# Optimization experiments

Measured on AMD Instinct MI355X. Metric: run time of the kernel, lower is better.

## Reference

```python
import jax, jax.numpy as jnp
import numpy as np

K, PAD, POOL = 3, 1, 2

def _conv_block(x, w, b):
    # x: [B,C,H,W]; w: [O, C*K*K] (Linear weight, feature order (C,kh,kw)); b: [O]
    O = w.shape[0]
    C = x.shape[1]
    ker = w.reshape(O, C, K, K)  # OIHW, matches torch unfold+linear ordering
    y = jax.lax.conv_general_dilated(
        x, ker, window_strides=(1, 1), padding=[(PAD, PAD), (PAD, PAD)],
        dimension_numbers=("NCHW", "OIHW", "NCHW"))
    y = y + b[None, :, None, None]
    y = jax.nn.relu(y)
    # non-overlapping max pool, drops remainder like torch unfold (sizes divisible here)
    y = jax.lax.reduce_window(y, -jnp.inf, jax.lax.max,
                              (1, 1, POOL, POOL), (1, 1, POOL, POOL), "VALID")
    return y

def setup_inputs() -> dict:
    key = jax.random.key(0)
    ks = jax.random.split(key, 9)
    B, Cin, H = 64, 3, 128
    C1, C2, FC, NCLS = 64, 128, 256, 1000
    flat = C2 * (H // 4) * (H // 4)  # 128*32*32 = 131072
    s = 0.05
    return {
        "x": jax.random.normal(ks[0], (B, Cin, H, H), jnp.float32),
        "conv1_w": jax.random.normal(ks[1], (C1, Cin * K * K), jnp.float32) * s,
        "conv1_b": jax.random.normal(ks[2], (C1,), jnp.float32) * s,
        "conv2_w": jax.random.normal(ks[3], (C2, C1 * K * K), jnp.float32) * s,
        "conv2_b": jax.random.normal(ks[4], (C2,), jnp.float32) * s,
        "fc1_w": jax.random.normal(ks[5], (FC, flat), jnp.float32) * 0.005,
        "fc1_b": jax.random.normal(ks[6], (FC,), jnp.float32) * s,
        "fc2_w": jax.random.normal(ks[7], (NCLS, FC), jnp.float32) * s,
        "fc2_b": jax.random.normal(ks[8], (NCLS,), jnp.float32) * s,
    }

def reference(x, conv1_w, conv1_b, conv2_w, conv2_b, fc1_w, fc1_b, fc2_w, fc2_b):
    h = _conv_block(x, conv1_w, conv1_b)      # [B,64,64,64]
    h = _conv_block(h, conv2_w, conv2_b)      # [B,128,32,32]
    h = h.reshape(h.shape[0], -1)             # NCHW flatten, same as torch .view
    h = jax.nn.relu(h @ fc1_w.T + fc1_b)
    return h @ fc2_w.T + fc2_b                # [B,1000]
```

## Files before the change

kernel.cpp:

```cpp
#include <hip/hip_runtime.h>
#include <hip/hip_bf16.h>

typedef __attribute__((ext_vector_type(8))) short short8;
typedef __attribute__((ext_vector_type(4))) float f32x4;

#define KFC   131072
#define NCLS  1000

__device__ __forceinline__ unsigned short f2bf(float f) {
  union { float f; unsigned u; } v; v.f = f;
  unsigned r = v.u + 0x7FFFu + ((v.u >> 16) & 1u);
  return (unsigned short)(r >> 16);
}

__device__ __forceinline__ unsigned pk2bf(float a, float b) {
  __hip_bfloat162 h = __float22bfloat162_rn(float2{a, b});
  union { __hip_bfloat162 h; unsigned u; } c; c.h = h;
  return c.u;
}

__global__ __launch_bounds__(256) void prep_w1(
    const float* __restrict__ w1, short* __restrict__ Bp1) {
  int i = blockIdx.x * 256 + threadIdx.x;
  int o = i >> 5, k = i & 31;
  Bp1[i] = (k < 27) ? (short)f2bf(w1[o * 27 + k]) : (short)0;
}

__global__ __launch_bounds__(256) void conv1_mfma(
    const float* __restrict__ x, const short* __restrict__ Bp1,
    const float* __restrict__ b1, unsigned short* __restrict__ y) {
  __shared__ unsigned short tile[1152];
  const int t = threadIdx.x;
  const int blk = blockIdx.x;
  const int tx = blk & 7, ty = (blk >> 3) & 7, b = blk >> 6;
  const int w = t >> 6, lane = t & 63;
  const int l15 = lane & 15, lg = lane >> 4;

  const int ih0 = ty * 16 - 1, iw0 = tx * 16 - 1;
  for (int i = t; i < 1152; i += 256) {
    unsigned short v = 0;
    if (i < 1080) {
      int ci = i / 360, rem = i - ci * 360;
      int tr = rem / 20, tc = rem - tr * 20;
      int ih = ih0 + tr, iw = iw0 + tc;
      if (tc < 18 && (unsigned)ih < 128u && (unsigned)iw < 128u)
        v = f2bf(x[(b * 3 + ci) * 16384 + (ih << 7) + iw]);
    }
    tile[i] = v;
  }

  short8 bf[4];
#pragma unroll
  for (int n = 0; n < 4; ++n)
    bf[n] = *(const short8*)(Bp1 + ((n * 16 + l15) << 5) + (lg << 3));

  int soff[8];
#pragma unroll
  for (int j = 0; j < 8; ++j) {
    int k = lg * 8 + j;
    if (k < 27) {
      int ci = k / 9, rem = k - ci * 9;
      int r = rem / 3, s = rem - r * 3;
      soff[j] = ci * 360 + r * 20 + s + l15 + w * 80;
    } else {
      soff[j] = 1080;
    }
  }
  __syncthreads();

  f32x4 acc[4][4];
#pragma unroll
  for (int m = 0; m < 4; ++m)
#pragma unroll
    for (int n = 0; n < 4; ++n) acc[m][n] = (f32x4){0.f, 0.f, 0.f, 0.f};

#pragma unroll
  for (int m = 0; m < 4; ++m) {
    union { short8 s; unsigned short u[8]; } af;
#pragma unroll
    for (int j = 0; j < 8; ++j) af.u[j] = tile[soff[j] + m * 20];
#pragma unroll
    for (int n = 0; n < 4; ++n)
      acc[m][n] = __builtin_amdgcn_mfma_f32_16x16x32_bf16(af.s, bf[n], acc[m][n], 0, 0, 0);
  }

#pragma unroll
  for (int n = 0; n < 4; ++n) {
    const int o = n * 16 + l15;
    const float bias = b1[o];
#pragma unroll
    for (int q = 0; q < 2; ++q) {
      const int pr = ty * 8 + w * 2 + q;
      float v0 = fmaxf(fmaxf(acc[2 * q][n][0], acc[2 * q][n][1]),
                       fmaxf(acc[2 * q + 1][n][0], acc[2 * q + 1][n][1]));
      float v1 = fmaxf(fmaxf(acc[2 * q][n][2], acc[2 * q][n][3]),
                       fmaxf(acc[2 * q + 1][n][2], acc[2 * q + 1][n][3]));
      v0 = fmaxf(v0 + bias, 0.f);
      v1 = fmaxf(v1 + bias, 0.f);
      const int pc = tx * 8 + lg * 2;
      unsigned short* dst = y + ((((size_t)b << 6) + pr) << 12) + ((size_t)pc << 6) + o;
      dst[0]  = f2bf(v0);
      dst[64] = f2bf(v1);
    }
  }
}

__global__ __launch_bounds__(256) void prep_w2(
    const float* __restrict__ w2, short* __restrict__ Bp) {
  int i = blockIdx.x * 256 + threadIdx.x;
  int c = i & 31, o = (i >> 5) & 127, pp = i >> 12;
  int cg = pp / 9, pos = pp - cg * 9;
  Bp[i] = (short)f2bf(w2[o * 576 + (cg * 32 + c) * 9 + pos]);
}

__global__ __launch_bounds__(512) void conv2_mfma(
    const short* __restrict__ yin, const short* __restrict__ Bp,
    const float* __restrict__ b2, unsigned int* __restrict__ A32) {
  __shared__ short tile[324 * 40];
  const int t = threadIdx.x;
  const int blk = blockIdx.x;
  const int tx = blk & 3, ty = (blk >> 2) & 3, b = blk >> 4;
  const int w = t >> 6, lane = t & 63;
  const int wm = w & 1, wn = w >> 1;
  const int l15 = lane & 15, lg = lane >> 4;

  f32x4 acc[8][2];
#pragma unroll
  for (int m = 0; m < 8; ++m)
#pragma unroll
    for (int n = 0; n < 2; ++n) acc[m][n] = (f32x4){0.f, 0.f, 0.f, 0.f};

  const int ih0 = ty * 16 - 1, iw0 = tx * 16 - 1;

#pragma unroll
  for (int cg = 0; cg < 2; ++cg) {
    __syncthreads();
    for (int i = t; i < 324 * 4; i += 512) {
      int p = i >> 2, q = i & 3;
      int sy = p / 18, sx = p - sy * 18;
      int ih = ih0 + sy, iw = iw0 + sx;
      short8 v = (short8){0, 0, 0, 0, 0, 0, 0, 0};
      if (((unsigned)ih < 64u) && ((unsigned)iw < 64u))
        v = *(const short8*)(yin + ((((size_t)b << 6) + ih) << 12) + ((size_t)iw << 6) + cg * 32 + q * 8);
      *(short8*)&tile[p * 40 + q * 8] = v;
    }
    __syncthreads();

    const int py0 = wm * 8;
#pragma unroll
    for (int pos = 0; pos < 9; ++pos) {
      const int kh = pos / 3, kw = pos % 3;
      short8 bf[2];
#pragma unroll
      for (int n = 0; n < 2; ++n)
        bf[n] = *(const short8*)(Bp + ((((cg * 9 + pos) << 7) + (wn * 2 + n) * 16 + l15) << 5) + (lg << 3));
#pragma unroll
      for (int half = 0; half < 2; ++half) {
        short8 af[4];
#pragma unroll
        for (int m = 0; m < 4; ++m) {
          int sy = py0 + half * 4 + m + kh, sx = l15 + kw;
          af[m] = *(const short8*)&tile[(sy * 18 + sx) * 40 + lg * 8];
        }
#pragma unroll
        for (int n = 0; n < 2; ++n)
#pragma unroll
          for (int m = 0; m < 4; ++m)
            acc[half * 4 + m][n] = __builtin_amdgcn_mfma_f32_16x16x32_bf16(af[m], bf[n], acc[half * 4 + m][n], 0, 0, 0);
      }
    }
  }

  const size_t bbase = ((size_t)b << 16);
#pragma unroll
  for (int n = 0; n < 2; ++n) {
    const int o = (wn * 2 + n) * 16 + l15;
    const float bias = b2[o];
#pragma unroll
    for (int mp = 0; mp < 4; ++mp) {
      const int prow = ty * 8 + wm * 4 + mp;
      float v0 = fmaxf(fmaxf(acc[2 * mp][n][0], acc[2 * mp][n][1]),
                       fmaxf(acc[2 * mp + 1][n][0], acc[2 * mp + 1][n][1]));
      float v1 = fmaxf(fmaxf(acc[2 * mp][n][2], acc[2 * mp][n][3]),
                       fmaxf(acc[2 * mp + 1][n][2], acc[2 * mp + 1][n][3]));
      v0 = fmaxf(v0 + bias, 0.f);
      v1 = fmaxf(v1 + bias, 0.f);
      unsigned pk = (unsigned)f2bf(v0) | ((unsigned)f2bf(v1) << 16);
      A32[bbase + (size_t)o * 512 + prow * 16 + tx * 4 + lg] = pk;
    }
  }
}

__global__ __launch_bounds__(256) void fc1_mfma(
    const unsigned short* __restrict__ A, const float* __restrict__ W,
    float* __restrict__ P) {
  __shared__ short Al[64][264];
  const int t = threadIdx.x;
  const int kc = blockIdx.x;
  const int wn = t >> 6, lane = t & 63;
  const int l15 = lane & 15, lg = lane >> 4;

  {
    const int row = t >> 2, q = t & 3;
    const unsigned short* asrc = A + (size_t)row * KFC + kc * 256 + q * 64;
    short8 ar[8];
#pragma unroll
    for (int i = 0; i < 8; ++i) ar[i] = *(const short8*)(asrc + i * 8);
#pragma unroll
    for (int i = 0; i < 8; ++i) *(short8*)&Al[row][q * 64 + i * 8] = ar[i];
  }
  __syncthreads();

  f32x4 acc[4][4];
#pragma unroll
  for (int m = 0; m < 4; ++m)
#pragma unroll
    for (int n = 0; n < 4; ++n) acc[m][n] = (f32x4){0.f, 0.f, 0.f, 0.f};

  const float* wrow[4];
#pragma unroll
  for (int n = 0; n < 4; ++n)
    wrow[n] = W + (size_t)(wn * 64 + n * 16 + l15) * KFC + kc * 256 + lg * 8;

#pragma unroll
  for (int ks = 0; ks < 8; ++ks) {
    short8 bf[4];
#pragma unroll
    for (int n = 0; n < 4; ++n) {
      f32x4 u = *(const f32x4*)(wrow[n] + ks * 32);
      f32x4 v = *(const f32x4*)(wrow[n] + ks * 32 + 4);
      union { short8 s; unsigned u32[4]; } pk;
      pk.u32[0] = pk2bf(u[0], u[1]);
      pk.u32[1] = pk2bf(u[2], u[3]);
      pk.u32[2] = pk2bf(v[0], v[1]);
      pk.u32[3] = pk2bf(v[2], v[3]);
      bf[n] = pk.s;
    }
    short8 af[4];
#pragma unroll
    for (int m = 0; m < 4; ++m)
      af[m] = *(const short8*)&Al[m * 16 + l15][ks * 32 + lg * 8];
#pragma unroll
    for (int n = 0; n < 4; ++n)
#pragma unroll
      for (int m = 0; m < 4; ++m)
        acc[m][n] = __builtin_amdgcn_mfma_f32_16x16x32_bf16(af[m], bf[n], acc[m][n], 0, 0, 0);
  }

  float* dst = P + (size_t)kc * 16384;
#pragma unroll
  for (int m = 0; m < 4; ++m)
#pragma unroll
    for (int n = 0; n < 4; ++n)
#pragma unroll
      for (int j = 0; j < 4; ++j) {
        int brow = m * 16 + lg * 4 + j;
        int o = wn * 64 + n * 16 + l15;
        dst[brow * 256 + o] = acc[m][n][j];
      }
}

__global__ __launch_bounds__(256) void fc1_reduce_kernel(
    const float* __restrict__ P, const float* __restrict__ fb1,
    float* __restrict__ Y) {
  __shared__ float red[4][64];
  const int t = threadIdx.x;
  const int iq = t & 63, pg = t >> 6;
  const int gidx = blockIdx.x * 64 + iq;
  const float* p0 = P + (size_t)(pg * 128) * 16384 + gidx;
  float s0 = 0, s1 = 0, s2 = 0, s3 = 0;
  for (int p = 0; p < 128; p += 4) {
    s0 += p0[(size_t)(p + 0) * 16384];
    s1 += p0[(size_t)(p + 1) * 16384];
    s2 += p0[(size_t)(p + 2) * 16384];
    s3 += p0[(size_t)(p + 3) * 16384];
  }
  red[pg][iq] = (s0 + s1) + (s2 + s3);
  __syncthreads();
  if (pg == 0) {
    float tot = (red[0][iq] + red[1][iq]) + (red[2][iq] + red[3][iq]);
    Y[gidx] = fmaxf(tot + fb1[gidx & 255], 0.f);
  }
}

__global__ __launch_bounds__(256) void fc2_kernel(
    const float* __restrict__ Y, const float* __restrict__ W2,
    const float* __restrict__ b2, float* __restrict__ out) {
  int tid = blockIdx.x * 256 + threadIdx.x;
  if (tid >= 64 * NCLS) return;
  int b = tid / NCLS, n = tid - b * NCLS;
  const float4* yv = (const float4*)(Y + b * 256);
  const float4* wv = (const float4*)(W2 + n * 256);
  float acc = 0.f;
#pragma unroll 8
  for (int f = 0; f < 64; ++f) {
    float4 a = yv[f], w = wv[f];
    acc += a.x * w.x + a.y * w.y + a.z * w.z + a.w * w.w;
  }
  out[tid] = acc + b2[n];
}

extern "C" void kernel_launch(void* const* d_in, const int* in_sizes, int n_in,
                              void* d_out, int out_size, void* d_ws, size_t ws_size,
                              hipStream_t stream) {
  const float* x   = (const float*)d_in[0];
  const float* w1  = (const float*)d_in[1];
  const float* b1  = (const float*)d_in[2];
  const float* w2  = (const float*)d_in[3];
  const float* b2  = (const float*)d_in[4];
  const float* fw1 = (const float*)d_in[5];
  const float* fb1 = (const float*)d_in[6];
  const float* fw2 = (const float*)d_in[7];
  const float* fb2 = (const float*)d_in[8];
  float* out = (float*)d_out;

  unsigned short* Y1 = (unsigned short*)d_ws;
  unsigned short* A16 = Y1 + 16777216;
  short* Bp = (short*)(A16 + 8388608);
  short* Bp1 = Bp + 73728;
  float* P  = (float*)(Bp1 + 2048);
  float* Yf = P + 8388608;

  prep_w2<<<288, 256, 0, stream>>>(w2, Bp);
  prep_w1<<<8, 256, 0, stream>>>(w1, Bp1);
  conv1_mfma<<<4096, 256, 0, stream>>>(x, Bp1, b1, Y1);
  conv2_mfma<<<1024, 512, 0, stream>>>((const short*)Y1, Bp, b2, (unsigned int*)A16);
  fc1_mfma<<<512, 256, 0, stream>>>(A16, fw1, P);
  fc1_reduce_kernel<<<256, 256, 0, stream>>>(P, fb1, Yf);
  fc2_kernel<<<250, 256, 0, stream>>>(Yf, fw2, fb2, out);
}
```

Before: 125.2 us.

## Halve conv2 tile height and double-buffer MFMA fragment loads

The conv2 kernel now uses 256-thread blocks covering an 8x16 output tile, with a smaller 10x18 shared halo tile and twice as many blocks. The inner loop is flattened into 18 steps that prefetch the next A and B fragments into double buffers while the current MFMAs run. The aim is to hide LDS and global load latency and to raise occupancy through lower LDS use. In exchange, halo re-reads grow because each tile is smaller, and register pressure rises from holding the extra buffers.

```diff
diff --git a/kernel.cpp b/kernel.cpp
--- a/kernel.cpp
+++ b/kernel.cpp
@@ -113,15 +113,14 @@
   Bp[i] = (short)f2bf(w2[o * 576 + (cg * 32 + c) * 9 + pos]);
 }
 
-__global__ __launch_bounds__(512) void conv2_mfma(
+__global__ __launch_bounds__(256) void conv2_mfma(
     const short* __restrict__ yin, const short* __restrict__ Bp,
     const float* __restrict__ b2, unsigned int* __restrict__ A32) {
-  __shared__ short tile[324 * 40];
+  __shared__ short tile[180 * 40];
   const int t = threadIdx.x;
   const int blk = blockIdx.x;
-  const int tx = blk & 3, ty = (blk >> 2) & 3, b = blk >> 4;
+  const int tx = blk & 3, ty = (blk >> 2) & 7, b = blk >> 5;
   const int w = t >> 6, lane = t & 63;
-  const int wm = w & 1, wn = w >> 1;
   const int l15 = lane & 15, lg = lane >> 4;
 
   f32x4 acc[8][2];
@@ -130,12 +129,13 @@
 #pragma unroll
     for (int n = 0; n < 2; ++n) acc[m][n] = (f32x4){0.f, 0.f, 0.f, 0.f};
 
-  const int ih0 = ty * 16 - 1, iw0 = tx * 16 - 1;
+  const int ih0 = ty * 8 - 1, iw0 = tx * 16 - 1;
+  const int abase = l15 * 40 + lg * 8;
 
 #pragma unroll
   for (int cg = 0; cg < 2; ++cg) {
     __syncthreads();
-    for (int i = t; i < 324 * 4; i += 512) {
+    for (int i = t; i < 180 * 4; i += 256) {
       int p = i >> 2, q = i & 3;
       int sy = p / 18, sx = p - sy * 18;
       int ih = ih0 + sy, iw = iw0 + sx;
@@ -146,39 +146,48 @@
     }
     __syncthreads();
 
-    const int py0 = wm * 8;
-#pragma unroll
-    for (int pos = 0; pos < 9; ++pos) {
-      const int kh = pos / 3, kw = pos % 3;
-      short8 bf[2];
+    short8 afb[2][4];
+    short8 bfb[2][2];
+
+#pragma unroll
+    for (int n = 0; n < 2; ++n)
+      bfb[0][n] = *(const short8*)(Bp + ((((cg * 9 + 0) << 7) + (w * 2 + n) * 16 + l15) << 5) + (lg << 3));
+#pragma unroll
+    for (int m = 0; m < 4; ++m)
+      afb[0][m] = *(const short8*)&tile[(m) * 18 * 40 + abase];
+
+#pragma unroll
+    for (int s = 0; s < 18; ++s) {
+      const int pos = s >> 1, half = s & 1;
+      if (s < 17) {
+        const int ns = s + 1, npos = ns >> 1, nhalf = ns & 1;
+        if (nhalf == 0) {
+#pragma unroll
+          for (int n = 0; n < 2; ++n)
+            bfb[npos & 1][n] = *(const short8*)(Bp + ((((cg * 9 + npos) << 7) + (w * 2 + n) * 16 + l15) << 5) + (lg << 3));
+        }
+        const int nkh = npos / 3, nkw = npos - nkh * 3;
+#pragma unroll
+        for (int m = 0; m < 4; ++m)
+          afb[ns & 1][m] = *(const short8*)&tile[(nhalf * 4 + m + nkh) * 18 * 40 + nkw * 40 + abase];
+      }
 #pragma unroll
       for (int n = 0; n < 2; ++n)
-        bf[n] = *(const short8*)(Bp + ((((cg * 9 + pos) << 7) + (wn * 2 + n) * 16 + l15) << 5) + (lg << 3));
-#pragma unroll
-      for (int half = 0; half < 2; ++half) {
-        short8 af[4];
-#pragma unroll
-        for (int m = 0; m < 4; ++m) {
-          int sy = py0 + half * 4 + m + kh, sx = l15 + kw;
-          af[m] = *(const short8*)&tile[(sy * 18 + sx) * 40 + lg * 8];
-        }
-#pragma unroll
-        for (int n = 0; n < 2; ++n)
-#pragma unroll
-          for (int m = 0; m < 4; ++m)
-            acc[half * 4 + m][n] = __builtin_amdgcn_mfma_f32_16x16x32_bf16(af[m], bf[n], acc[half * 4 + m][n], 0, 0, 0);
-      }
+#pragma unroll
+        for (int m = 0; m < 4; ++m)
+          acc[half * 4 + m][n] = __builtin_amdgcn_mfma_f32_16x16x32_bf16(
+              afb[s & 1][m], bfb[pos & 1][n], acc[half * 4 + m][n], 0, 0, 0);
     }
   }
 
   const size_t bbase = ((size_t)b << 16);
 #pragma unroll
   for (int n = 0; n < 2; ++n) {
-    const int o = (wn * 2 + n) * 16 + l15;
+    const int o = (w * 2 + n) * 16 + l15;
     const float bias = b2[o];
 #pragma unroll
     for (int mp = 0; mp < 4; ++mp) {
-      const int prow = ty * 8 + wm * 4 + mp;
+      const int prow = ty * 4 + mp;
       float v0 = fmaxf(fmaxf(acc[2 * mp][n][0], acc[2 * mp][n][1]),
                        fmaxf(acc[2 * mp + 1][n][0], acc[2 * mp + 1][n][1]));
       float v1 = fmaxf(fmaxf(acc[2 * mp][n][2], acc[2 * mp][n][3]),
@@ -324,7 +333,7 @@
   prep_w2<<<288, 256, 0, stream>>>(w2, Bp);
   prep_w1<<<8, 256, 0, stream>>>(w1, Bp1);
   conv1_mfma<<<4096, 256, 0, stream>>>(x, Bp1, b1, Y1);
-  conv2_mfma<<<1024, 512, 0, stream>>>((const short*)Y1, Bp, b2, (unsigned int*)A16);
+  conv2_mfma<<<2048, 256, 0, stream>>>((const short*)Y1, Bp, b2, (unsigned int*)A16);
   fc1_mfma<<<512, 256, 0, stream>>>(A16, fw1, P);
   fc1_reduce_kernel<<<256, 256, 0, stream>>>(P, fb1, Yf);
   fc2_kernel<<<250, 256, 0, stream>>>(Yf, fw2, fb2, out);
```

Result: faster. 120.1 us (-4.1%).
